# Kernel optimization log

Hardware: AMD Instinct MI355X
Metric: run time of the kernel (lower is better)

The kernel has to match this reference:

```python
import jax, jax.numpy as jnp
import numpy as np

N = 50000
E = 800000
NFEAT = 256
NHID = 64
HEADS = 4
NCLASS = 16
NEG_SLOPE = 0.2


def setup_inputs() -> dict:
    key = jax.random.key(0)
    ks = jax.random.split(key, 12)
    g = lambda k, s, scale: (jax.random.normal(k, s, dtype=jnp.float32) * scale)
    inp = {
        "x": g(ks[0], (N, NFEAT), 1.0),
        "src": jax.random.randint(ks[1], (E,), 0, N, dtype=jnp.int32),
        "dst": jax.random.randint(ks[2], (E,), 0, N, dtype=jnp.int32),
        # layer 1 params (DGL GATConv: fc no-bias, attn_l/attn_r, output bias)
        "W1": g(ks[3], (NFEAT, HEADS * NHID), (2.0 / NFEAT) ** 0.5),
        "al1": g(ks[4], (HEADS, NHID), 0.1),
        "ar1": g(ks[5], (HEADS, NHID), 0.1),
        "b1": jnp.zeros((HEADS * NHID,), dtype=jnp.float32),
        # layer 2 params (1 head)
        "W2": g(ks[6], (HEADS * NHID, NCLASS), (2.0 / (HEADS * NHID)) ** 0.5),
        "al2": g(ks[7], (1, NCLASS), 0.1),
        "ar2": g(ks[8], (1, NCLASS), 0.1),
        "b2": jnp.zeros((NCLASS,), dtype=jnp.float32),
    }
    return inp


def gat_conv(x, src, dst, W, al, ar, b, heads, dh):
    # x: [N, Fin] -> feat: [N, H, D]
    n = x.shape[0]
    feat = (x @ W).reshape(n, heads, dh)
    el = jnp.einsum("nhd,hd->nh", feat, al)  # [N, H]
    er = jnp.einsum("nhd,hd->nh", feat, ar)
    e = jax.nn.leaky_relu(el[src] + er[dst], NEG_SLOPE)  # [E, H]
    # segment softmax over destination nodes
    emax = jax.ops.segment_max(e, dst, num_segments=n)
    emax = jnp.where(jnp.isfinite(emax), emax, jnp.float32(0.0))
    ex = jnp.exp(e - emax[dst])  # [E, H]
    denom = jax.ops.segment_sum(ex, dst, num_segments=n)  # [N, H]
    alpha = ex / denom[dst]  # [E, H]
    # gather src feats, weight, scatter-add to dst
    msg = feat[src] * alpha[:, :, None]  # [E, H, D]
    out = jax.ops.segment_sum(msg, dst, num_segments=n)  # [N, H, D]
    return out + b.reshape(1, heads, dh)


def reference(x, src, dst, W1, al1, ar1, b1, W2, al2, ar2, b2):
    h = gat_conv(x, src, dst, W1, al1, ar1, b1, HEADS, NHID)  # [N, 4, nhid]
    h = h.reshape(N, HEADS * NHID)
    h = jax.nn.elu(h)
    h = gat_conv(h, src, dst, W2, al2, ar2, b2, 1, NCLASS)  # [N, 1, nclass]
    h = h.reshape(N, NCLASS)
    return jax.nn.log_softmax(h, axis=1)
```

## Files before the change

kernel.cpp:

```cpp
#include <hip/hip_runtime.h>
#include <hip/hip_bf16.h>

#define N_NODES 50000
#define NP1     50001
#define N_EDGES 800000
#define NFEAT   256
#define NHID    64
#define HEADS   4
#define NCLASS  16
#define NEG_SLOPE 0.2f

#define NBLK  782
#define NBUCK 196
#define NSCAN (NBUCK * NBLK)
#define NSCB  150

typedef __attribute__((ext_vector_type(8))) short short8;
typedef __attribute__((ext_vector_type(4))) float floatx4;

__device__ __forceinline__ float blo(unsigned int u) { return __uint_as_float(u << 16); }
__device__ __forceinline__ float bhi(unsigned int u) { return __uint_as_float(u & 0xffff0000u); }
__device__ __forceinline__ unsigned short f2b(float f) {
    unsigned int x = __float_as_uint(f);
    unsigned int r = x + 0x7fffu + ((x >> 16) & 1u);
    return (unsigned short)(r >> 16);
}
__device__ __forceinline__ unsigned int pack2(float a, float b) {
    return (unsigned int)f2b(a) | ((unsigned int)f2b(b) << 16);
}
__device__ __forceinline__ float leaky(float x) { return fmaxf(x, NEG_SLOPE * x); }

__global__ __launch_bounds__(256) void p1_kernel(
        const int* __restrict__ dst, int* __restrict__ bhist,
        const float* __restrict__ W1, const float* __restrict__ W2,
        const float* __restrict__ al1, const float* __restrict__ ar1,
        unsigned short* __restrict__ W1E, unsigned short* __restrict__ W2T) {
    __shared__ float tile[64][65];
    __shared__ int hist[NBUCK];
    int b = blockIdx.x, t = threadIdx.x;
    if (b < NBLK) {
        if (t < NBUCK) hist[t] = 0;
        __syncthreads();
        int e = (b * 256 + t) * 4;
        if (e < N_EDGES) {
            int4 d = *(const int4*)&dst[e];
            atomicAdd(&hist[d.x >> 8], 1);
            atomicAdd(&hist[d.y >> 8], 1);
            atomicAdd(&hist[d.z >> 8], 1);
            atomicAdd(&hist[d.w >> 8], 1);
        }
        __syncthreads();
        if (t < NBUCK) bhist[t * NBLK + b] = hist[t];
        return;
    }
    int pb = b - NBLK;
    if (pb < 16) {
        int tk = (pb & 3) * 64, tn = (pb >> 2) * 64;
        int tx = t & 63, ty = t >> 6;
#pragma unroll
        for (int r = 0; r < 16; ++r) {
            int row = ty * 16 + r;
            tile[row][tx] = W1[(tk + row) * 256 + tn + tx];
        }
        __syncthreads();
#pragma unroll
        for (int r = 0; r < 16; ++r) {
            int row = ty * 16 + r;
            W1E[(tn + row) * 256 + tk + tx] = f2b(tile[tx][row]);
        }
    } else if (pb < 20) {
        int h = pb - 16;
        int w = t >> 6, lane = t & 63;
        float alv = al1[h * 64 + lane];
        float arv = ar1[h * 64 + lane];
        for (int k = w; k < 256; k += 4) {
            float wv = W1[k * 256 + h * 64 + lane];
            float sl = wv * alv, sr = wv * arv;
#pragma unroll
            for (int off = 1; off < 64; off <<= 1) {
                sl += __shfl_xor(sl, off);
                sr += __shfl_xor(sr, off);
            }
            if (lane == 0) {
                W1E[(256 + h) * 256 + k] = f2b(sl);
                W1E[(260 + h) * 256 + k] = f2b(sr);
            }
        }
    } else {
        int n = t >> 4, k0 = (t & 15) * 16;
#pragma unroll
        for (int j = 0; j < 16; ++j)
            W2T[n * 256 + k0 + j] = f2b(W2[(k0 + j) * 16 + n]);
#pragma unroll
        for (int j = 0; j < 8; ++j)
            W1E[264 * 256 + j * 256 + t] = 0;
    }
}

__global__ __launch_bounds__(256) void scanA_kernel(const int* __restrict__ bhist,
                                                    int* __restrict__ partial,
                                                    int* __restrict__ bsum) {
    __shared__ int wsum[4];
    int t = threadIdx.x;
    int base = blockIdx.x * 1024 + t * 4;
    int v0 = (base + 0 < NSCAN) ? bhist[base + 0] : 0;
    int v1 = (base + 1 < NSCAN) ? bhist[base + 1] : 0;
    int v2 = (base + 2 < NSCAN) ? bhist[base + 2] : 0;
    int v3 = (base + 3 < NSCAN) ? bhist[base + 3] : 0;
    int s = v0 + v1 + v2 + v3;
    int lane = t & 63, w = t >> 6;
    int incl = s;
#pragma unroll
    for (int off = 1; off < 64; off <<= 1) {
        int x = __shfl_up(incl, off);
        if (lane >= off) incl += x;
    }
    if (lane == 63) wsum[w] = incl;
    __syncthreads();
    int woff = 0;
    for (int k = 0; k < w; ++k) woff += wsum[k];
    int excl = woff + incl - s;
    if (base + 0 < NSCAN) partial[base + 0] = excl;
    if (base + 1 < NSCAN) partial[base + 1] = excl + v0;
    if (base + 2 < NSCAN) partial[base + 2] = excl + v0 + v1;
    if (base + 3 < NSCAN) partial[base + 3] = excl + v0 + v1 + v2;
    if (t == 255) bsum[blockIdx.x] = woff + incl;
}

__global__ __launch_bounds__(256) void scanB_kernel(const int* __restrict__ partial,
                                                    const int* __restrict__ bsum,
                                                    int* __restrict__ scanned) {
    __shared__ int wsum[4];
    __shared__ int sb[256];
    int t = threadIdx.x;
    int v = (t < NSCB) ? bsum[t] : 0;
    int lane = t & 63, w = t >> 6;
    int incl = v;
#pragma unroll
    for (int off = 1; off < 64; off <<= 1) {
        int x = __shfl_up(incl, off);
        if (lane >= off) incl += x;
    }
    if (lane == 63) wsum[w] = incl;
    __syncthreads();
    int woff = 0;
    for (int k = 0; k < w; ++k) woff += wsum[k];
    sb[t] = woff + incl - v;
    __syncthreads();
    int base = blockIdx.x * 1024 + t * 4;
#pragma unroll
    for (int j = 0; j < 4; ++j) {
        int i = base + j;
        if (i < NSCAN) scanned[i] = partial[i] + sb[i >> 10];
    }
}

__global__ __launch_bounds__(256) void p2_kernel(const int* __restrict__ src,
                                                 const int* __restrict__ dst,
                                                 const int* __restrict__ scanned,
                                                 int* __restrict__ ebuf) {
    __shared__ int bs[NBUCK];
    int b = blockIdx.x, t = threadIdx.x;
    if (t < NBUCK) bs[t] = scanned[t * NBLK + b];
    __syncthreads();
    int e = (b * 256 + t) * 4;
    if (e < N_EDGES) {
        int4 d = *(const int4*)&dst[e];
        int4 s = *(const int4*)&src[e];
        int p0 = atomicAdd(&bs[d.x >> 8], 1);
        ebuf[p0] = (s.x << 8) | (d.x & 255);
        int p1 = atomicAdd(&bs[d.y >> 8], 1);
        ebuf[p1] = (s.y << 8) | (d.y & 255);
        int p2 = atomicAdd(&bs[d.z >> 8], 1);
        ebuf[p2] = (s.z << 8) | (d.z & 255);
        int p3 = atomicAdd(&bs[d.w >> 8], 1);
        ebuf[p3] = (s.w << 8) | (d.w & 255);
    }
}

__global__ __launch_bounds__(256) void p3_kernel(const int* __restrict__ scanned,
                                                 const int* __restrict__ ebuf,
                                                 int* __restrict__ row_ptr,
                                                 int* __restrict__ csr_src) {
    __shared__ int lcnt[256];
    __shared__ int loff[256];
    __shared__ int wsum[4];
    int b = blockIdx.x, t = threadIdx.x;
    int base = scanned[b * NBLK];
    int endb = (b == NBUCK - 1) ? N_EDGES : scanned[(b + 1) * NBLK];
    lcnt[t] = 0;
    __syncthreads();
    for (int i = base + t; i < endb; i += 256)
        atomicAdd(&lcnt[ebuf[i] & 255], 1);
    __syncthreads();
    int v = lcnt[t];
    int lane = t & 63, w = t >> 6;
    int incl = v;
#pragma unroll
    for (int off = 1; off < 64; off <<= 1) {
        int x = __shfl_up(incl, off);
        if (lane >= off) incl += x;
    }
    if (lane == 63) wsum[w] = incl;
    __syncthreads();
    int woff = 0;
    for (int k = 0; k < w; ++k) woff += wsum[k];
    int excl = woff + incl - v;
    loff[t] = base + excl;
    int node = b * 256 + t;
    if (node < NP1) row_ptr[node] = base + excl;
    if (b == NBUCK - 1 && t == 255) row_ptr[N_NODES] = N_EDGES;
    __syncthreads();
    for (int i = base + t; i < endb; i += 256) {
        int p = ebuf[i];
        int pos = atomicAdd(&loff[p & 255], 1);
        csr_src[pos] = p >> 8;
    }
}

__global__ __launch_bounds__(256, 2) void gemm1_mfma_kernel(
        const float* __restrict__ X, const unsigned short* __restrict__ BT,
        unsigned short* __restrict__ C, float* __restrict__ el, float* __restrict__ er) {
    __shared__ __align__(16) unsigned short As[128 * 40];
    __shared__ __align__(16) unsigned short Bs[272 * 40];
    int t = threadIdx.x;
    int m0 = blockIdx.x * 128;
    int lane = t & 63, wm = t >> 6;
    int quad = lane >> 4, l16 = lane & 15;

    floatx4 acc[2][17];
#pragma unroll
    for (int i = 0; i < 2; ++i)
#pragma unroll
        for (int j = 0; j < 17; ++j) acc[i][j] = (floatx4){0.f, 0.f, 0.f, 0.f};

    int arow = t >> 1, ak = (t & 1) * 16;
    int grow = m0 + arow;
    const float* xrow = X + (size_t)grow * 256 + ak;

    for (int k0 = 0; k0 < 256; k0 += 32) {
        float4 v0 = make_float4(0.f, 0.f, 0.f, 0.f), v1 = v0, v2 = v0, v3 = v0;
        if (grow < N_NODES) {
            v0 = *(const float4*)(xrow + k0 + 0);
            v1 = *(const float4*)(xrow + k0 + 4);
            v2 = *(const float4*)(xrow + k0 + 8);
            v3 = *(const float4*)(xrow + k0 + 12);
        }
        uint4 p0, p1;
        p0.x = pack2(v0.x, v0.y); p0.y = pack2(v0.z, v0.w);
        p0.z = pack2(v1.x, v1.y); p0.w = pack2(v1.z, v1.w);
        p1.x = pack2(v2.x, v2.y); p1.y = pack2(v2.z, v2.w);
        p1.z = pack2(v3.x, v3.y); p1.w = pack2(v3.z, v3.w);
        *(uint4*)&As[arow * 40 + ak] = p0;
        *(uint4*)&As[arow * 40 + ak + 8] = p1;
#pragma unroll
        for (int i = 0; i < 5; ++i) {
            int ch = t + i * 256;
            if (ch < 1088) {
                int row = ch >> 2, off = (ch & 3) * 8;
                *(uint4*)&Bs[row * 40 + off] = *(const uint4*)(BT + row * 256 + k0 + off);
            }
        }
        __syncthreads();

        short8 a0 = *(const short8*)&As[(wm * 32 + l16) * 40 + quad * 8];
        short8 a1 = *(const short8*)&As[(wm * 32 + 16 + l16) * 40 + quad * 8];
#pragma unroll
        for (int nf = 0; nf < 17; ++nf) {
            short8 bb = *(const short8*)&Bs[(nf * 16 + l16) * 40 + quad * 8];
            acc[0][nf] = __builtin_amdgcn_mfma_f32_16x16x32_bf16(a0, bb, acc[0][nf], 0, 0, 0);
            acc[1][nf] = __builtin_amdgcn_mfma_f32_16x16x32_bf16(a1, bb, acc[1][nf], 0, 0, 0);
        }
        __syncthreads();
    }

#pragma unroll
    for (int mf = 0; mf < 2; ++mf) {
#pragma unroll
        for (int r = 0; r < 4; ++r) {
            int row = m0 + wm * 32 + mf * 16 + quad * 4 + r;
            if (row < N_NODES && l16 < 8) {
                float v = acc[mf][16][r];
                if (l16 < 4) el[row * 4 + l16] = v;
                else er[row * 4 + (l16 - 4)] = v;
            }
        }
    }

    unsigned short* scr = Bs + wm * 1536;
    int half = lane >> 5, l32 = lane & 31;
    int rrow = l32 >> 1, coff = (l32 & 1) * 8;
#pragma unroll
    for (int mf = 0; mf < 2; ++mf) {
#pragma unroll
        for (int p = 0; p < 8; ++p) {
            unsigned short* base = scr + (p & 1) * 768;
#pragma unroll
            for (int fr = 0; fr < 2; ++fr) {
                int nf = 2 * p + fr;
                unsigned short* fb = base + fr * 384;
#pragma unroll
                for (int r = 0; r < 4; ++r)
                    fb[(quad * 4 + r) * 24 + l16] = f2b(acc[mf][nf][r]);
            }
            uint4 val = *(const uint4*)(base + half * 384 + rrow * 24 + coff);
            int row = m0 + wm * 32 + mf * 16 + rrow;
            int nf = 2 * p + half;
            if (row < N_NODES)
                *(uint4*)&C[(size_t)row * 256 + nf * 16 + coff] = val;
        }
    }
}

__global__ void agg1_kernel(const unsigned short* __restrict__ feat1,
                            const float* __restrict__ el, const float* __restrict__ er,
                            const int* __restrict__ row_ptr, const int* __restrict__ csr_src,
                            const float* __restrict__ b1, unsigned short* __restrict__ h1b) {
    int wave = threadIdx.x >> 6, lane = threadIdx.x & 63;
    int n = blockIdx.x * 4 + wave;
    if (n >= N_NODES) return;
    int q = lane >> 4, l16 = lane & 15;
    int h = l16 >> 2;
    float er_h = er[n * 4 + h];
    int start = row_ptr[n], end = row_ptr[n + 1];

    float acc[16];
#pragma unroll
    for (int j = 0; j < 16; ++j) acc[j] = 0.f;
    float denom = 0.f;

    int i = start + q;
    for (; i + 4 < end; i += 8) {
        int s0 = csr_src[i];
        int s1 = csr_src[i + 4];
        float ex0 = __expf(leaky(el[s0 * 4 + h] + er_h));
        float ex1 = __expf(leaky(el[s1 * 4 + h] + er_h));
        const uint4* p0 = (const uint4*)(feat1 + (size_t)s0 * 256 + l16 * 16);
        const uint4* p1 = (const uint4*)(feat1 + (size_t)s1 * 256 + l16 * 16);
        uint4 a0 = p0[0], a1 = p0[1];
        uint4 b0 = p1[0], b1v = p1[1];
        denom += ex0 + ex1;
        acc[0]  = fmaf(blo(a0.x), ex0, acc[0]);   acc[0]  = fmaf(blo(b0.x), ex1, acc[0]);
        acc[1]  = fmaf(bhi(a0.x), ex0, acc[1]);   acc[1]  = fmaf(bhi(b0.x), ex1, acc[1]);
        acc[2]  = fmaf(blo(a0.y), ex0, acc[2]);   acc[2]  = fmaf(blo(b0.y), ex1, acc[2]);
        acc[3]  = fmaf(bhi(a0.y), ex0, acc[3]);   acc[3]  = fmaf(bhi(b0.y), ex1, acc[3]);
        acc[4]  = fmaf(blo(a0.z), ex0, acc[4]);   acc[4]  = fmaf(blo(b0.z), ex1, acc[4]);
        acc[5]  = fmaf(bhi(a0.z), ex0, acc[5]);   acc[5]  = fmaf(bhi(b0.z), ex1, acc[5]);
        acc[6]  = fmaf(blo(a0.w), ex0, acc[6]);   acc[6]  = fmaf(blo(b0.w), ex1, acc[6]);
        acc[7]  = fmaf(bhi(a0.w), ex0, acc[7]);   acc[7]  = fmaf(bhi(b0.w), ex1, acc[7]);
        acc[8]  = fmaf(blo(a1.x), ex0, acc[8]);   acc[8]  = fmaf(blo(b1v.x), ex1, acc[8]);
        acc[9]  = fmaf(bhi(a1.x), ex0, acc[9]);   acc[9]  = fmaf(bhi(b1v.x), ex1, acc[9]);
        acc[10] = fmaf(blo(a1.y), ex0, acc[10]);  acc[10] = fmaf(blo(b1v.y), ex1, acc[10]);
        acc[11] = fmaf(bhi(a1.y), ex0, acc[11]);  acc[11] = fmaf(bhi(b1v.y), ex1, acc[11]);
        acc[12] = fmaf(blo(a1.z), ex0, acc[12]);  acc[12] = fmaf(blo(b1v.z), ex1, acc[12]);
        acc[13] = fmaf(bhi(a1.z), ex0, acc[13]);  acc[13] = fmaf(bhi(b1v.z), ex1, acc[13]);
        acc[14] = fmaf(blo(a1.w), ex0, acc[14]);  acc[14] = fmaf(blo(b1v.w), ex1, acc[14]);
        acc[15] = fmaf(bhi(a1.w), ex0, acc[15]);  acc[15] = fmaf(bhi(b1v.w), ex1, acc[15]);
    }
    if (i < end) {
        int s = csr_src[i];
        float ex = __expf(leaky(el[s * 4 + h] + er_h));
        const uint4* p = (const uint4*)(feat1 + (size_t)s * 256 + l16 * 16);
        uint4 u0 = p[0], u1 = p[1];
        denom += ex;
        acc[0]  = fmaf(blo(u0.x), ex, acc[0]);
        acc[1]  = fmaf(bhi(u0.x), ex, acc[1]);
        acc[2]  = fmaf(blo(u0.y), ex, acc[2]);
        acc[3]  = fmaf(bhi(u0.y), ex, acc[3]);
        acc[4]  = fmaf(blo(u0.z), ex, acc[4]);
        acc[5]  = fmaf(bhi(u0.z), ex, acc[5]);
        acc[6]  = fmaf(blo(u0.w), ex, acc[6]);
        acc[7]  = fmaf(bhi(u0.w), ex, acc[7]);
        acc[8]  = fmaf(blo(u1.x), ex, acc[8]);
        acc[9]  = fmaf(bhi(u1.x), ex, acc[9]);
        acc[10] = fmaf(blo(u1.y), ex, acc[10]);
        acc[11] = fmaf(bhi(u1.y), ex, acc[11]);
        acc[12] = fmaf(blo(u1.z), ex, acc[12]);
        acc[13] = fmaf(bhi(u1.z), ex, acc[13]);
        acc[14] = fmaf(blo(u1.w), ex, acc[14]);
        acc[15] = fmaf(bhi(u1.w), ex, acc[15]);
    }
#pragma unroll
    for (int j = 0; j < 16; ++j) {
        acc[j] += __shfl_xor(acc[j], 16);
        acc[j] += __shfl_xor(acc[j], 32);
    }
    denom += __shfl_xor(denom, 16);
    denom += __shfl_xor(denom, 32);

    if (q == 0) {
        float inv = (end > start) ? 1.f / denom : 0.f;
        float o[16];
#pragma unroll
        for (int j = 0; j < 16; j += 4) {
            float4 b4 = *(const float4*)&b1[l16 * 16 + j];
            o[j + 0] = fmaf(acc[j + 0], inv, b4.x);
            o[j + 1] = fmaf(acc[j + 1], inv, b4.y);
            o[j + 2] = fmaf(acc[j + 2], inv, b4.z);
            o[j + 3] = fmaf(acc[j + 3], inv, b4.w);
        }
#pragma unroll
        for (int j = 0; j < 16; ++j) o[j] = o[j] > 0.f ? o[j] : __expf(o[j]) - 1.f;
        uint4 pa, pb;
        pa.x = pack2(o[0], o[1]);   pa.y = pack2(o[2], o[3]);
        pa.z = pack2(o[4], o[5]);   pa.w = pack2(o[6], o[7]);
        pb.x = pack2(o[8], o[9]);   pb.y = pack2(o[10], o[11]);
        pb.z = pack2(o[12], o[13]); pb.w = pack2(o[14], o[15]);
        uint4* dstp = (uint4*)(h1b + (size_t)n * 256 + l16 * 16);
        dstp[0] = pa;
        dstp[1] = pb;
    }
}

__global__ __launch_bounds__(256) void gemm2_mfma_kernel(
        const unsigned short* __restrict__ h1b, const unsigned short* __restrict__ W2T,
        const float* __restrict__ al2, const float* __restrict__ ar2,
        float* __restrict__ feat2, float* __restrict__ el2, float* __restrict__ er2) {
    int wave = threadIdx.x >> 6, lane = threadIdx.x & 63;
    int l16 = lane & 15, quad = lane >> 4;
    int row0 = (blockIdx.x * 4 + wave) * 16;
    if (row0 >= N_NODES) return;
    floatx4 acc = (floatx4){0.f, 0.f, 0.f, 0.f};
    const unsigned short* arow = h1b + (size_t)(row0 + l16) * 256 + quad * 8;
    const unsigned short* brow = W2T + (size_t)l16 * 256 + quad * 8;
#pragma unroll
    for (int k0 = 0; k0 < 256; k0 += 32) {
        short8 a = *(const short8*)(arow + k0);
        short8 b = *(const short8*)(brow + k0);
        acc = __builtin_amdgcn_mfma_f32_16x16x32_bf16(a, b, acc, 0, 0, 0);
    }
    float a2 = al2[l16], r2 = ar2[l16];
#pragma unroll
    for (int r = 0; r < 4; ++r) {
        int row = row0 + quad * 4 + r;
        float v = acc[r];
        feat2[row * 16 + l16] = v;
        float pl = v * a2, pr = v * r2;
#pragma unroll
        for (int off = 1; off < 16; off <<= 1) {
            pl += __shfl_xor(pl, off);
            pr += __shfl_xor(pr, off);
        }
        if (l16 == 0) {
            el2[row] = pl;
            er2[row] = pr;
        }
    }
}

__global__ void agg2_kernel(const float* __restrict__ feat2, const float* __restrict__ el2,
                            const float* __restrict__ er2, const int* __restrict__ row_ptr,
                            const int* __restrict__ csr_src, const float* __restrict__ b2,
                            float* __restrict__ out) {
    int wave = threadIdx.x >> 6, lane = threadIdx.x & 63;
    int n = blockIdx.x * 4 + wave;
    if (n >= N_NODES) return;
    int start = row_ptr[n], end = row_ptr[n + 1];
    float ern = er2[n];
    int eo = lane >> 4, c = lane & 15;
    float acc = 0.f, denom = 0.f;
    int i = start + eo;
    for (; i + 4 < end; i += 8) {
        int s0 = csr_src[i], s1 = csr_src[i + 4];
        float ex0 = __expf(leaky(el2[s0] + ern));
        float ex1 = __expf(leaky(el2[s1] + ern));
        float f0 = feat2[s0 * 16 + c], f1 = feat2[s1 * 16 + c];
        denom += ex0 + ex1;
        acc = fmaf(f0, ex0, acc);
        acc = fmaf(f1, ex1, acc);
    }
    if (i < end) {
        int s = csr_src[i];
        float ex = __expf(leaky(el2[s] + ern));
        denom += ex;
        acc = fmaf(feat2[s * 16 + c], ex, acc);
    }
    acc += __shfl_xor(acc, 16);
    acc += __shfl_xor(acc, 32);
    denom += __shfl_xor(denom, 16);
    denom += __shfl_xor(denom, 32);
    float v = ((end > start) ? acc / denom : 0.f) + b2[c];
    float mx = v;
#pragma unroll
    for (int off = 1; off < 16; off <<= 1) mx = fmaxf(mx, __shfl_xor(mx, off));
    float ex2 = __expf(v - mx);
    float s2 = ex2;
#pragma unroll
    for (int off = 1; off < 16; off <<= 1) s2 += __shfl_xor(s2, off);
    float res = v - mx - logf(s2);
    if (lane < 16) out[n * 16 + lane] = res;
}

extern "C" void kernel_launch(void* const* d_in, const int* in_sizes, int n_in,
                              void* d_out, int out_size, void* d_ws, size_t ws_size,
                              hipStream_t stream) {
    const float* x   = (const float*)d_in[0];
    const int*   src = (const int*)d_in[1];
    const int*   dst = (const int*)d_in[2];
    const float* W1  = (const float*)d_in[3];
    const float* al1 = (const float*)d_in[4];
    const float* ar1 = (const float*)d_in[5];
    const float* b1  = (const float*)d_in[6];
    const float* W2  = (const float*)d_in[7];
    const float* al2 = (const float*)d_in[8];
    const float* ar2 = (const float*)d_in[9];
    const float* b2  = (const float*)d_in[10];
    float* out = (float*)d_out;

    char* ws = (char*)d_ws;
    size_t off = 0;
    auto alloc = [&](size_t bytes) -> void* {
        void* p = ws + off;
        off += (bytes + 255) & ~(size_t)255;
        return p;
    };
    unsigned short* W1E   = (unsigned short*)alloc((size_t)272 * 256 * 2);
    unsigned short* W2T   = (unsigned short*)alloc((size_t)16 * 256 * 2);
    unsigned short* feat1 = (unsigned short*)alloc((size_t)N_NODES * 256 * 2);
    unsigned short* h1b   = (unsigned short*)alloc((size_t)N_NODES * 256 * 2);
    float* feat2   = (float*)alloc((size_t)N_NODES * 16 * 4);
    float* el1     = (float*)alloc((size_t)N_NODES * 4 * 4);
    float* er1     = (float*)alloc((size_t)N_NODES * 4 * 4);
    float* el2     = (float*)alloc((size_t)N_NODES * 4);
    float* er2     = (float*)alloc((size_t)N_NODES * 4);
    int*   bhist   = (int*)alloc((size_t)NSCAN * 4);
    int*   partial = (int*)alloc((size_t)NSCAN * 4);
    int*   scanned = (int*)alloc((size_t)NSCAN * 4);
    int*   bsum    = (int*)alloc((size_t)256 * 4);
    int*   row_ptr = (int*)alloc((size_t)NP1 * 4);
    int*   ebuf    = (int*)alloc((size_t)N_EDGES * 4);
    int*   csr_src = (int*)alloc((size_t)N_EDGES * 4);

    dim3 b256(256);
    p1_kernel<<<NBLK + 21, b256, 0, stream>>>(dst, bhist, W1, W2, al1, ar1, W1E, W2T);
    scanA_kernel<<<NSCB, b256, 0, stream>>>(bhist, partial, bsum);
    scanB_kernel<<<NSCB, b256, 0, stream>>>(partial, bsum, scanned);
    p2_kernel<<<NBLK, b256, 0, stream>>>(src, dst, scanned, ebuf);
    p3_kernel<<<NBUCK, b256, 0, stream>>>(scanned, ebuf, row_ptr, csr_src);

    gemm1_mfma_kernel<<<(N_NODES + 127) / 128, b256, 0, stream>>>(x, W1E, feat1, el1, er1);
    agg1_kernel<<<(N_NODES + 3) / 4, b256, 0, stream>>>(feat1, el1, er1, row_ptr, csr_src, b1, h1b);

    gemm2_mfma_kernel<<<(N_NODES + 63) / 64, b256, 0, stream>>>(h1b, W2T, al2, ar2, feat2, el2, er2);
    agg2_kernel<<<(N_NODES + 3) / 4, b256, 0, stream>>>(feat2, el2, er2, row_ptr, csr_src, b2, out);
}
```

Baseline: 276.9 us.

## Store layer-1 features as FP8 and fold second scan pass into consumers

The layer-1 projected features are now written as FP8 (e4m3 via cvt_pk_fp8) instead of bf16, halving the bytes gathered per edge in the layer-1 aggregation, which is unpacked with cvt_pk_f32_fp8. Separately, the scanB kernel is removed and each p2/p3 block recomputes the block-sum prefix locally, saving a launch and a global round-trip. FP8 storage reduces feature precision and may hurt accuracy tolerance. The explicit row_ptr[N] store was dropped, relying on node index N being covered by the last bucket.

```diff
diff --git a/kernel.cpp b/kernel.cpp
--- a/kernel.cpp
+++ b/kernel.cpp
@@ -17,6 +17,7 @@
 
 typedef __attribute__((ext_vector_type(8))) short short8;
 typedef __attribute__((ext_vector_type(4))) float floatx4;
+typedef __attribute__((ext_vector_type(2))) float floatx2;
 
 __device__ __forceinline__ float blo(unsigned int u) { return __uint_as_float(u << 16); }
 __device__ __forceinline__ float bhi(unsigned int u) { return __uint_as_float(u & 0xffff0000u); }
@@ -29,6 +30,18 @@
     return (unsigned int)f2b(a) | ((unsigned int)f2b(b) << 16);
 }
 __device__ __forceinline__ float leaky(float x) { return fmaxf(x, NEG_SLOPE * x); }
+
+__device__ __forceinline__ void fp8acc(uint4 u, float ex, float* acc) {
+    floatx2 p;
+    p = __builtin_amdgcn_cvt_pk_f32_fp8(u.x, 0); acc[0]  = fmaf(p[0], ex, acc[0]);  acc[1]  = fmaf(p[1], ex, acc[1]);
+    p = __builtin_amdgcn_cvt_pk_f32_fp8(u.x, 1); acc[2]  = fmaf(p[0], ex, acc[2]);  acc[3]  = fmaf(p[1], ex, acc[3]);
+    p = __builtin_amdgcn_cvt_pk_f32_fp8(u.y, 0); acc[4]  = fmaf(p[0], ex, acc[4]);  acc[5]  = fmaf(p[1], ex, acc[5]);
+    p = __builtin_amdgcn_cvt_pk_f32_fp8(u.y, 1); acc[6]  = fmaf(p[0], ex, acc[6]);  acc[7]  = fmaf(p[1], ex, acc[7]);
+    p = __builtin_amdgcn_cvt_pk_f32_fp8(u.z, 0); acc[8]  = fmaf(p[0], ex, acc[8]);  acc[9]  = fmaf(p[1], ex, acc[9]);
+    p = __builtin_amdgcn_cvt_pk_f32_fp8(u.z, 1); acc[10] = fmaf(p[0], ex, acc[10]); acc[11] = fmaf(p[1], ex, acc[11]);
+    p = __builtin_amdgcn_cvt_pk_f32_fp8(u.w, 0); acc[12] = fmaf(p[0], ex, acc[12]); acc[13] = fmaf(p[1], ex, acc[13]);
+    p = __builtin_amdgcn_cvt_pk_f32_fp8(u.w, 1); acc[14] = fmaf(p[0], ex, acc[14]); acc[15] = fmaf(p[1], ex, acc[15]);
+}
 
 __global__ __launch_bounds__(256) void p1_kernel(
         const int* __restrict__ dst, int* __restrict__ bhist,
@@ -127,41 +140,35 @@
     if (t == 255) bsum[blockIdx.x] = woff + incl;
 }
 
-__global__ __launch_bounds__(256) void scanB_kernel(const int* __restrict__ partial,
-                                                    const int* __restrict__ bsum,
-                                                    int* __restrict__ scanned) {
+__global__ __launch_bounds__(256) void p2_kernel(const int* __restrict__ src,
+                                                 const int* __restrict__ dst,
+                                                 const int* __restrict__ partial,
+                                                 const int* __restrict__ bsum,
+                                                 int* __restrict__ ebuf) {
     __shared__ int wsum[4];
     __shared__ int sb[256];
-    int t = threadIdx.x;
-    int v = (t < NSCB) ? bsum[t] : 0;
-    int lane = t & 63, w = t >> 6;
-    int incl = v;
-#pragma unroll
-    for (int off = 1; off < 64; off <<= 1) {
-        int x = __shfl_up(incl, off);
-        if (lane >= off) incl += x;
-    }
-    if (lane == 63) wsum[w] = incl;
-    __syncthreads();
-    int woff = 0;
-    for (int k = 0; k < w; ++k) woff += wsum[k];
-    sb[t] = woff + incl - v;
-    __syncthreads();
-    int base = blockIdx.x * 1024 + t * 4;
-#pragma unroll
-    for (int j = 0; j < 4; ++j) {
-        int i = base + j;
-        if (i < NSCAN) scanned[i] = partial[i] + sb[i >> 10];
-    }
-}
-
-__global__ __launch_bounds__(256) void p2_kernel(const int* __restrict__ src,
-                                                 const int* __restrict__ dst,
-                                                 const int* __restrict__ scanned,
-                                                 int* __restrict__ ebuf) {
     __shared__ int bs[NBUCK];
     int b = blockIdx.x, t = threadIdx.x;
-    if (t < NBUCK) bs[t] = scanned[t * NBLK + b];
+    {
+        int v = (t < NSCB) ? bsum[t] : 0;
+        int lane = t & 63, w = t >> 6;
+        int incl = v;
+#pragma unroll
+        for (int off = 1; off < 64; off <<= 1) {
+            int x = __shfl_up(incl, off);
+            if (lane >= off) incl += x;
+        }
+        if (lane == 63) wsum[w] = incl;
+        __syncthreads();
+        int woff = 0;
+        for (int k = 0; k < w; ++k) woff += wsum[k];
+        sb[t] = woff + incl - v;
+    }
+    __syncthreads();
+    if (t < NBUCK) {
+        int idx = t * NBLK + b;
+        bs[t] = partial[idx] + sb[idx >> 10];
+    }
     __syncthreads();
     int e = (b * 256 + t) * 4;
     if (e < N_EDGES) {
@@ -178,16 +185,40 @@
     }
 }
 
-__global__ __launch_bounds__(256) void p3_kernel(const int* __restrict__ scanned,
+__global__ __launch_bounds__(256) void p3_kernel(const int* __restrict__ partial,
+                                                 const int* __restrict__ bsum,
                                                  const int* __restrict__ ebuf,
                                                  int* __restrict__ row_ptr,
                                                  int* __restrict__ csr_src) {
     __shared__ int lcnt[256];
     __shared__ int loff[256];
     __shared__ int wsum[4];
+    __shared__ int sb[256];
     int b = blockIdx.x, t = threadIdx.x;
-    int base = scanned[b * NBLK];
-    int endb = (b == NBUCK - 1) ? N_EDGES : scanned[(b + 1) * NBLK];
+    {
+        int v = (t < NSCB) ? bsum[t] : 0;
+        int lane = t & 63, w = t >> 6;
+        int incl = v;
+#pragma unroll
+        for (int off = 1; off < 64; off <<= 1) {
+            int x = __shfl_up(incl, off);
+            if (lane >= off) incl += x;
+        }
+        if (lane == 63) wsum[w] = incl;
+        __syncthreads();
+        int woff = 0;
+        for (int k = 0; k < w; ++k) woff += wsum[k];
+        sb[t] = woff + incl - v;
+    }
+    __syncthreads();
+    int i0 = b * NBLK;
+    int base = partial[i0] + sb[i0 >> 10];
+    int endb;
+    if (b == NBUCK - 1) endb = N_EDGES;
+    else {
+        int i1 = (b + 1) * NBLK;
+        endb = partial[i1] + sb[i1 >> 10];
+    }
     lcnt[t] = 0;
     __syncthreads();
     for (int i = base + t; i < endb; i += 256)
@@ -209,7 +240,6 @@
     loff[t] = base + excl;
     int node = b * 256 + t;
     if (node < NP1) row_ptr[node] = base + excl;
-    if (b == NBUCK - 1 && t == 255) row_ptr[N_NODES] = N_EDGES;
     __syncthreads();
     for (int i = base + t; i < endb; i += 256) {
         int p = ebuf[i];
@@ -220,7 +250,7 @@
 
 __global__ __launch_bounds__(256, 2) void gemm1_mfma_kernel(
         const float* __restrict__ X, const unsigned short* __restrict__ BT,
-        unsigned short* __restrict__ C, float* __restrict__ el, float* __restrict__ er) {
+        unsigned char* __restrict__ C, float* __restrict__ el, float* __restrict__ er) {
     __shared__ __align__(16) unsigned short As[128 * 40];
     __shared__ __align__(16) unsigned short Bs[272 * 40];
     int t = threadIdx.x;
@@ -306,13 +336,23 @@
             uint4 val = *(const uint4*)(base + half * 384 + rrow * 24 + coff);
             int row = m0 + wm * 32 + mf * 16 + rrow;
             int nf = 2 * p + half;
-            if (row < N_NODES)
-                *(uint4*)&C[(size_t)row * 256 + nf * 16 + coff] = val;
-        }
-    }
-}
-
-__global__ void agg1_kernel(const unsigned short* __restrict__ feat1,
+            if (row < N_NODES) {
+                float f0 = blo(val.x), f1 = bhi(val.x), f2 = blo(val.y), f3 = bhi(val.y);
+                float f4 = blo(val.z), f5 = bhi(val.z), f6 = blo(val.w), f7 = bhi(val.w);
+                int lo = __builtin_amdgcn_cvt_pk_fp8_f32(f0, f1, 0, 0);
+                lo = __builtin_amdgcn_cvt_pk_fp8_f32(f2, f3, lo, 1);
+                int hi = __builtin_amdgcn_cvt_pk_fp8_f32(f4, f5, 0, 0);
+                hi = __builtin_amdgcn_cvt_pk_fp8_f32(f6, f7, hi, 1);
+                uint2 o;
+                o.x = (unsigned int)lo;
+                o.y = (unsigned int)hi;
+                *(uint2*)&C[(size_t)row * 256 + nf * 16 + coff] = o;
+            }
+        }
+    }
+}
+
+__global__ void agg1_kernel(const unsigned char* __restrict__ feat1,
                             const float* __restrict__ el, const float* __restrict__ er,
                             const int* __restrict__ row_ptr, const int* __restrict__ csr_src,
                             const float* __restrict__ b1, unsigned short* __restrict__ h1b) {
@@ -335,50 +375,18 @@
         int s1 = csr_src[i + 4];
         float ex0 = __expf(leaky(el[s0 * 4 + h] + er_h));
         float ex1 = __expf(leaky(el[s1 * 4 + h] + er_h));
-        const uint4* p0 = (const uint4*)(feat1 + (size_t)s0 * 256 + l16 * 16);
-        const uint4* p1 = (const uint4*)(feat1 + (size_t)s1 * 256 + l16 * 16);
-        uint4 a0 = p0[0], a1 = p0[1];
-        uint4 b0 = p1[0], b1v = p1[1];
+        uint4 a = *(const uint4*)(feat1 + (size_t)s0 * 256 + l16 * 16);
+        uint4 b = *(const uint4*)(feat1 + (size_t)s1 * 256 + l16 * 16);
         denom += ex0 + ex1;
-        acc[0]  = fmaf(blo(a0.x), ex0, acc[0]);   acc[0]  = fmaf(blo(b0.x), ex1, acc[0]);
-        acc[1]  = fmaf(bhi(a0.x), ex0, acc[1]);   acc[1]  = fmaf(bhi(b0.x), ex1, acc[1]);
-        acc[2]  = fmaf(blo(a0.y), ex0, acc[2]);   acc[2]  = fmaf(blo(b0.y), ex1, acc[2]);
-        acc[3]  = fmaf(bhi(a0.y), ex0, acc[3]);   acc[3]  = fmaf(bhi(b0.y), ex1, acc[3]);
-        acc[4]  = fmaf(blo(a0.z), ex0, acc[4]);   acc[4]  = fmaf(blo(b0.z), ex1, acc[4]);
-        acc[5]  = fmaf(bhi(a0.z), ex0, acc[5]);   acc[5]  = fmaf(bhi(b0.z), ex1, acc[5]);
-        acc[6]  = fmaf(blo(a0.w), ex0, acc[6]);   acc[6]  = fmaf(blo(b0.w), ex1, acc[6]);
-        acc[7]  = fmaf(bhi(a0.w), ex0, acc[7]);   acc[7]  = fmaf(bhi(b0.w), ex1, acc[7]);
-        acc[8]  = fmaf(blo(a1.x), ex0, acc[8]);   acc[8]  = fmaf(blo(b1v.x), ex1, acc[8]);
-        acc[9]  = fmaf(bhi(a1.x), ex0, acc[9]);   acc[9]  = fmaf(bhi(b1v.x), ex1, acc[9]);
-        acc[10] = fmaf(blo(a1.y), ex0, acc[10]);  acc[10] = fmaf(blo(b1v.y), ex1, acc[10]);
-        acc[11] = fmaf(bhi(a1.y), ex0, acc[11]);  acc[11] = fmaf(bhi(b1v.y), ex1, acc[11]);
-        acc[12] = fmaf(blo(a1.z), ex0, acc[12]);  acc[12] = fmaf(blo(b1v.z), ex1, acc[12]);
-        acc[13] = fmaf(bhi(a1.z), ex0, acc[13]);  acc[13] = fmaf(bhi(b1v.z), ex1, acc[13]);
-        acc[14] = fmaf(blo(a1.w), ex0, acc[14]);  acc[14] = fmaf(blo(b1v.w), ex1, acc[14]);
-        acc[15] = fmaf(bhi(a1.w), ex0, acc[15]);  acc[15] = fmaf(bhi(b1v.w), ex1, acc[15]);
+        fp8acc(a, ex0, acc);
+        fp8acc(b, ex1, acc);
     }
     if (i < end) {
         int s = csr_src[i];
         float ex = __expf(leaky(el[s * 4 + h] + er_h));
-        const uint4* p = (const uint4*)(feat1 + (size_t)s * 256 + l16 * 16);
-        uint4 u0 = p[0], u1 = p[1];
+        uint4 u = *(const uint4*)(feat1 + (size_t)s * 256 + l16 * 16);
         denom += ex;
-        acc[0]  = fmaf(blo(u0.x), ex, acc[0]);
-        acc[1]  = fmaf(bhi(u0.x), ex, acc[1]);
-        acc[2]  = fmaf(blo(u0.y), ex, acc[2]);
-        acc[3]  = fmaf(bhi(u0.y), ex, acc[3]);
-        acc[4]  = fmaf(blo(u0.z), ex, acc[4]);
-        acc[5]  = fmaf(bhi(u0.z), ex, acc[5]);
-        acc[6]  = fmaf(blo(u0.w), ex, acc[6]);
-        acc[7]  = fmaf(bhi(u0.w), ex, acc[7]);
-        acc[8]  = fmaf(blo(u1.x), ex, acc[8]);
-        acc[9]  = fmaf(bhi(u1.x), ex, acc[9]);
-        acc[10] = fmaf(blo(u1.y), ex, acc[10]);
-        acc[11] = fmaf(bhi(u1.y), ex, acc[11]);
-        acc[12] = fmaf(blo(u1.z), ex, acc[12]);
-        acc[13] = fmaf(bhi(u1.z), ex, acc[13]);
-        acc[14] = fmaf(blo(u1.w), ex, acc[14]);
-        acc[15] = fmaf(bhi(u1.w), ex, acc[15]);
+        fp8acc(u, ex, acc);
     }
 #pragma unroll
     for (int j = 0; j < 16; ++j) {
@@ -516,7 +524,7 @@
     };
     unsigned short* W1E   = (unsigned short*)alloc((size_t)272 * 256 * 2);
     unsigned short* W2T   = (unsigned short*)alloc((size_t)16 * 256 * 2);
-    unsigned short* feat1 = (unsigned short*)alloc((size_t)N_NODES * 256 * 2);
+    unsigned char*  feat1 = (unsigned char*)alloc((size_t)N_NODES * 256);
     unsigned short* h1b   = (unsigned short*)alloc((size_t)N_NODES * 256 * 2);
     float* feat2   = (float*)alloc((size_t)N_NODES * 16 * 4);
     float* el1     = (float*)alloc((size_t)N_NODES * 4 * 4);
@@ -525,7 +533,6 @@
     float* er2     = (float*)alloc((size_t)N_NODES * 4);
     int*   bhist   = (int*)alloc((size_t)NSCAN * 4);
     int*   partial = (int*)alloc((size_t)NSCAN * 4);
-    int*   scanned = (int*)alloc((size_t)NSCAN * 4);
     int*   bsum    = (int*)alloc((size_t)256 * 4);
     int*   row_ptr = (int*)alloc((size_t)NP1 * 4);
     int*   ebuf    = (int*)alloc((size_t)N_EDGES * 4);
@@ -534,9 +541,8 @@
     dim3 b256(256);
     p1_kernel<<<NBLK + 21, b256, 0, stream>>>(dst, bhist, W1, W2, al1, ar1, W1E, W2T);
     scanA_kernel<<<NSCB, b256, 0, stream>>>(bhist, partial, bsum);
-    scanB_kernel<<<NSCB, b256, 0, stream>>>(partial, bsum, scanned);
-    p2_kernel<<<NBLK, b256, 0, stream>>>(src, dst, scanned, ebuf);
-    p3_kernel<<<NBUCK, b256, 0, stream>>>(scanned, ebuf, row_ptr, csr_src);
+    p2_kernel<<<NBLK, b256, 0, stream>>>(src, dst, partial, bsum, ebuf);
+    p3_kernel<<<NBUCK, b256, 0, stream>>>(partial, bsum, ebuf, row_ptr, csr_src);
 
     gemm1_mfma_kernel<<<(N_NODES + 127) / 128, b256, 0, stream>>>(x, W1E, feat1, el1, er1);
     agg1_kernel<<<(N_NODES + 3) / 4, b256, 0, stream>>>(feat1, el1, er1, row_ptr, csr_src, b1, h1b);
```

Result: faster. 253.1 us (-8.6%).
